# Optimization experiments

Measured on AMD Instinct MI355X. Metric: run time of the kernel, lower is better.

## Reference

```python
import jax, jax.numpy as jnp
import numpy as np

N_ITER = 2          # GenSP n_iter
M_COEF = 0.0        # GenSP M (positional-feature weight)
AFF_SOFTMAX = 1.0   # GenSP affinity_softmax


def setup_inputs() -> dict:
    key = jax.random.key(0)
    x = jax.random.normal(key, (2, 64, 256, 256), dtype=jnp.float32)
    return {"x": x, "stoken_size": 16}


def reference(x, stoken_size):
    # Faithful JAX version of GenSP.forward / ssn_iter (softmax_order='v0',
    # ws=None -> ws=2*stride0-1, i.e. each pixel searches its 9 neighboring
    # superpixel centroids; dist_type='l2' squared distance).
    B, C, H, W = x.shape
    s = int(stoken_size)
    nH, nW = (H - 1) // s + 1, (W - 1) // s + 1
    nS = nH * nW
    N = H * W

    # append_grid: concat scaled (y,x) coordinate channels, scale = M/stride0
    scale = jnp.asarray(M_COEF / s, x.dtype)
    gy, gx = jnp.meshgrid(jnp.arange(H, dtype=x.dtype) * scale,
                          jnp.arange(W, dtype=x.dtype) * scale, indexing='ij')
    grid = jnp.broadcast_to(jnp.stack([gy, gx])[None], (B, 2, H, W))
    feats = jnp.concatenate([x, grid], axis=1)          # [B, C+2, H, W]
    C2 = C + 2
    pf = feats.reshape(B, C2, N)                        # pixel features

    # calc_init_centroid: adaptive_avg_pool2d to (nH, nW); H,W divisible by s
    cent = feats.reshape(B, C2, nH, s, nW, s).mean(axis=(3, 5)).reshape(B, C2, nS)

    # per-pixel base superpixel cell and its 3x3 candidate neighborhood
    yy, xx = jnp.meshgrid(jnp.arange(H), jnp.arange(W), indexing='ij')
    sy = (yy // s).reshape(-1)                          # [N]
    sx = (xx // s).reshape(-1)
    dy, dx = jnp.meshgrid(jnp.arange(-1, 2), jnp.arange(-1, 2), indexing='ij')
    dy = dy.reshape(-1); dx = dx.reshape(-1)            # [9]
    cy = sy[:, None] + dy[None]                         # [N, 9]
    cx = sx[:, None] + dx[None]
    valid = (cy >= 0) & (cy < nH) & (cx >= 0) & (cx < nW)
    cand = jnp.where(valid, cy * nW + cx, 0)            # candidate spixel ids
    pix = jnp.broadcast_to(jnp.arange(N)[:, None], (N, 9))
    flat = (cand * N + pix).reshape(-1)                 # [9N] flat COO index
    NEG = jnp.asarray(-1e30, x.dtype)

    affinity = None
    for it in range(N_ITER):
        ck = cent[:, :, cand]                           # [B, C2, N, 9] gather
        d = jnp.sum((pf[:, :, :, None] - ck) ** 2, axis=1)  # squared-l2 [B,N,9]
        logits = jnp.where(valid[None], -AFF_SOFTMAX * d, NEG)
        w = jax.nn.softmax(logits, axis=-1)             # softmax_order 'v0'
        w = jnp.where(valid[None], w, jnp.asarray(0.0, x.dtype))
        # sparse-COO -> dense scatter: A[b, spix, pix] = w
        A = jnp.zeros((B, nS * N), x.dtype).at[:, flat].add(w.reshape(B, -1))
        affinity = A.reshape(B, nS, N)
        if it < N_ITER - 1:
            # spixel_features = bmm(A, pf^T) / (A.sum(2) + 1e-16)
            num = jnp.einsum('bsn,bcn->bcs', affinity, pf)
            den = affinity.sum(axis=2)[:, None] + 1e-16
            cent = num / den
    return affinity
```

## Files before the change

kernel.cpp:

```cpp
#include <hip/hip_runtime.h>
#include <cstdint>


#define WDIM   256
#define NPIX   65536
#define NSUP   256
#define OUT_F4 8388608u
#define WS_Z_F4 8320u

__device__ __forceinline__ unsigned short f2bf(float f) {
    unsigned u = __float_as_uint(f);
    u = (u + 0x7FFFu + ((u >> 16) & 1u)) >> 16;
    return (unsigned short)u;
}
__device__ __forceinline__ float bf2f(unsigned short h) {
    return __uint_as_float(((unsigned)h) << 16);
}

__global__ __launch_bounds__(256) void kfill(float4* __restrict__ out4,
                                             float4* __restrict__ ws4) {
    unsigned idx = blockIdx.x * 256u + threadIdx.x;
    float4 z = make_float4(0.f, 0.f, 0.f, 0.f);
    if (idx < OUT_F4) {
        out4[idx] = z;
    } else {
        unsigned k = idx - OUT_F4;
        if (k < WS_Z_F4) ws4[8192u + k] = z;
    }
}

__global__ __launch_bounds__(256) void kcent0(const float* __restrict__ x,
                                              float* __restrict__ cent0) {
    __shared__ float red[64];
    int blk = blockIdx.x;
    int b  = blk >> 10;
    int c  = (blk >> 4) & 63;
    int sy = blk & 15;
    const float4* s4 = (const float4*)(x + (((size_t)b << 22) | ((size_t)c << 16) | ((size_t)sy << 12)));
    int u = threadIdx.x;
    float4 a0 = s4[u], a1 = s4[u + 256], a2 = s4[u + 512], a3 = s4[u + 768];
    float p = (a0.x + a0.y + a0.z + a0.w) + (a1.x + a1.y + a1.z + a1.w)
            + (a2.x + a2.y + a2.z + a2.w) + (a3.x + a3.y + a3.z + a3.w);
    p += __shfl_xor(p, 1, 64);
    p += __shfl_xor(p, 2, 64);
    int lane = u & 63, wv = u >> 6;
    if ((lane & 3) == 0) red[wv * 16 + (lane >> 2)] = p;
    __syncthreads();
    if (u < 16) {
        float v = (red[u] + red[16 + u] + red[32 + u] + red[48 + u]) * (1.0f / 256.0f);
        cent0[(((b << 8) | (sy << 4) | u) << 6) + c] = v;
    }
}

__global__ __launch_bounds__(256) void kiter0(const float* __restrict__ x,
                                              const float* __restrict__ cent0,
                                              float* __restrict__ num,
                                              float* __restrict__ den) {
    __shared__ __align__(16) float smem[12544];
    float* w_lds = smem;
    unsigned short* pS = (unsigned short*)(smem + 3072);
    float* part = smem + 3072;

    int blk = blockIdx.x;
    int b = blk >> 8, sidx = blk & 255;
    int sy = sidx >> 4, sx = sidx & 15;
    int t  = threadIdx.x;
    int py = t >> 4, px = t & 15;
    int n  = ((sy << 4) + py) * WDIM + (sx << 4) + px;
    const float* xp = x + ((size_t)b << 22) + n;
    const float* cb = cent0 + ((size_t)b << 14);

    int candj[9]; bool valj[9];
#pragma unroll
    for (int j = 0; j < 9; j++) {
        int cy = sy + j / 3 - 1, cx = sx + j % 3 - 1;
        bool v = (cy >= 0) && (cy < 16) && (cx >= 0) && (cx < 16);
        valj[j] = v;
        candj[j] = v ? ((cy << 4) | cx) : 0;
    }

    float d[9];
#pragma unroll
    for (int j = 0; j < 9; j++) d[j] = 0.f;

#pragma unroll 8
    for (int cq = 0; cq < 32; cq++) {
        float pc0 = xp[(size_t)(2 * cq) << 16];
        float pc1 = xp[(size_t)(2 * cq + 1) << 16];
#pragma unroll
        for (int j = 0; j < 9; j++) {
            float c0 = cb[(candj[j] << 6) + 2 * cq];
            float c1 = cb[(candj[j] << 6) + 2 * cq + 1];
            float f0 = pc0 - c0, f1 = pc1 - c1;
            d[j] = fmaf(f0, f0, d[j]);
            d[j] = fmaf(f1, f1, d[j]);
        }
        *(ushort2*)&pS[t * 70 + 2 * cq] = make_ushort2(f2bf(pc0), f2bf(pc1));
    }

    float M = -1e30f;
#pragma unroll
    for (int j = 0; j < 9; j++) if (valj[j]) M = fmaxf(M, -d[j]);
    float w[9], Z = 0.f;
#pragma unroll
    for (int j = 0; j < 9; j++) { w[j] = valj[j] ? __expf(-d[j] - M) : 0.f; Z += w[j]; }
    float rZ = 1.0f / Z;
#pragma unroll
    for (int j = 0; j < 9; j++) { w[j] *= rZ; w_lds[t * 12 + j] = w[j]; }

    __syncthreads();

    int tg = t >> 4, cg = t & 15;
    float acc[9][4];
    float dacc[9];
#pragma unroll
    for (int j = 0; j < 9; j++) {
        dacc[j] = 0.f;
        acc[j][0] = 0.f; acc[j][1] = 0.f; acc[j][2] = 0.f; acc[j][3] = 0.f;
    }
#pragma unroll 4
    for (int i = 0; i < 16; i++) {
        int tt = (tg << 4) + i;
        float4 wA = *(const float4*)&w_lds[tt * 12];
        float4 wB = *(const float4*)&w_lds[tt * 12 + 4];
        float  w8 = w_lds[tt * 12 + 8];
        ushort2 A2 = *(const ushort2*)&pS[tt * 70 + 4 * cg];
        ushort2 B2 = *(const ushort2*)&pS[tt * 70 + 4 * cg + 2];
        float p0 = bf2f(A2.x), p1 = bf2f(A2.y), p2v = bf2f(B2.x), p3v = bf2f(B2.y);
        float ww[9] = {wA.x, wA.y, wA.z, wA.w, wB.x, wB.y, wB.z, wB.w, w8};
#pragma unroll
        for (int j = 0; j < 9; j++) {
            dacc[j] += ww[j];
            acc[j][0] = fmaf(ww[j], p0, acc[j][0]);
            acc[j][1] = fmaf(ww[j], p1, acc[j][1]);
            acc[j][2] = fmaf(ww[j], p2v, acc[j][2]);
            acc[j][3] = fmaf(ww[j], p3v, acc[j][3]);
        }
    }

    __syncthreads();

#pragma unroll
    for (int j = 0; j < 9; j++)
        *(float4*)&part[tg * 592 + (j << 6) + (cg << 2)] =
            make_float4(acc[j][0], acc[j][1], acc[j][2], acc[j][3]);
    if (cg == 0) {
#pragma unroll
        for (int j = 0; j < 9; j++) part[tg * 592 + 576 + j] = dacc[j];
    }

    __syncthreads();

    for (int o = t; o < 585; o += 256) {
        float s = 0.f;
#pragma unroll
        for (int tg2 = 0; tg2 < 16; tg2++) s += part[tg2 * 592 + o];
        if (o < 576) {
            int j = o >> 6, c = o & 63;
            int cy = sy + j / 3 - 1, cx = sx + j % 3 - 1;
            if (cy >= 0 && cy < 16 && cx >= 0 && cx < 16)
                atomicAdd(&num[((size_t)((b << 8) | (cy << 4) | cx) << 6) + c], s);
        } else {
            int j = o - 576;
            int cy = sy + j / 3 - 1, cx = sx + j % 3 - 1;
            if (cy >= 0 && cy < 16 && cx >= 0 && cx < 16)
                atomicAdd(&den[(b << 8) | (cy << 4) | cx], s);
        }
    }
}

__global__ __launch_bounds__(256) void kdiv(const float* __restrict__ num,
                                            const float* __restrict__ den,
                                            float* __restrict__ cent1) {
    int i = blockIdx.x * 256 + threadIdx.x;
    cent1[i] = num[i] / (den[i >> 6] + 1e-16f);
}

__global__ __launch_bounds__(256) void kiter1(const float* __restrict__ x,
                                              const float* __restrict__ cent1,
                                              float* __restrict__ out) {
    int blk = blockIdx.x;
    int b = blk >> 8, sidx = blk & 255;
    int sy = sidx >> 4, sx = sidx & 15;
    int t  = threadIdx.x;
    int py = t >> 4, px = t & 15;
    int n  = ((sy << 4) + py) * WDIM + (sx << 4) + px;
    const float* xp = x + ((size_t)b << 22) + n;
    const float* cb = cent1 + ((size_t)b << 14);

    int candj[9]; bool valj[9];
#pragma unroll
    for (int j = 0; j < 9; j++) {
        int cy = sy + j / 3 - 1, cx = sx + j % 3 - 1;
        bool v = (cy >= 0) && (cy < 16) && (cx >= 0) && (cx < 16);
        valj[j] = v;
        candj[j] = v ? ((cy << 4) | cx) : 0;
    }

    float d[9];
#pragma unroll
    for (int j = 0; j < 9; j++) d[j] = 0.f;

#pragma unroll 8
    for (int cq = 0; cq < 32; cq++) {
        float pc0 = xp[(size_t)(2 * cq) << 16];
        float pc1 = xp[(size_t)(2 * cq + 1) << 16];
#pragma unroll
        for (int j = 0; j < 9; j++) {
            float c0 = cb[(candj[j] << 6) + 2 * cq];
            float c1 = cb[(candj[j] << 6) + 2 * cq + 1];
            float f0 = pc0 - c0, f1 = pc1 - c1;
            d[j] = fmaf(f0, f0, d[j]);
            d[j] = fmaf(f1, f1, d[j]);
        }
    }

    float M = -1e30f;
#pragma unroll
    for (int j = 0; j < 9; j++) if (valj[j]) M = fmaxf(M, -d[j]);
    float w[9], Z = 0.f;
#pragma unroll
    for (int j = 0; j < 9; j++) { w[j] = valj[j] ? __expf(-d[j] - M) : 0.f; Z += w[j]; }
    float rZ = 1.0f / Z;

    float* ob = out + ((size_t)b << 24) + n;
#pragma unroll
    for (int j = 0; j < 9; j++)
        if (valj[j]) ob[(size_t)candj[j] << 16] = w[j] * rZ;
}

extern "C" void kernel_launch(void* const* d_in, const int* in_sizes, int n_in,
                              void* d_out, int out_size, void* d_ws, size_t ws_size,
                              hipStream_t stream) {
    (void)in_sizes; (void)n_in; (void)out_size; (void)ws_size;
    const float* x = (const float*)d_in[0];
    float* out = (float*)d_out;
    float* ws  = (float*)d_ws;
    float* cent0 = ws;
    float* num   = ws + 32768;
    float* den   = ws + 65536;
    float* cent1 = ws + 66048;

    kfill <<<32801, 256, 0, stream>>>((float4*)out, (float4*)ws);
    kcent0<<<2048,  256, 0, stream>>>(x, cent0);
    kiter0<<<512,   256, 0, stream>>>(x, cent0, num, den);
    kdiv  <<<128,   256, 0, stream>>>(num, den, cent1);
    kiter1<<<512,   256, 0, stream>>>(x, cent1, out);
}
```

Baseline: 189.5 us.

## Replace zero-fill plus scatter with compact weights and single dense expand pass

Result: no change. 189.3 us (-0.1%).

```diff
diff --git a/kernel.cpp b/kernel.cpp
--- a/kernel.cpp
+++ b/kernel.cpp
@@ -1,12 +1,6 @@
 #include <hip/hip_runtime.h>
 #include <cstdint>
 
-
-#define WDIM   256
-#define NPIX   65536
-#define NSUP   256
-#define OUT_F4 8388608u
-#define WS_Z_F4 8320u
 
 __device__ __forceinline__ unsigned short f2bf(float f) {
     unsigned u = __float_as_uint(f);
@@ -17,27 +11,17 @@
     return __uint_as_float(((unsigned)h) << 16);
 }
 
-__global__ __launch_bounds__(256) void kfill(float4* __restrict__ out4,
-                                             float4* __restrict__ ws4) {
-    unsigned idx = blockIdx.x * 256u + threadIdx.x;
-    float4 z = make_float4(0.f, 0.f, 0.f, 0.f);
-    if (idx < OUT_F4) {
-        out4[idx] = z;
-    } else {
-        unsigned k = idx - OUT_F4;
-        if (k < WS_Z_F4) ws4[8192u + k] = z;
-    }
-}
-
 __global__ __launch_bounds__(256) void kcent0(const float* __restrict__ x,
-                                              float* __restrict__ cent0) {
+                                              float* __restrict__ cent0,
+                                              float* __restrict__ numden) {
     __shared__ float red[64];
     int blk = blockIdx.x;
+    int u = threadIdx.x;
+    if (blk < 130) numden[blk * 256 + u] = 0.f;
     int b  = blk >> 10;
     int c  = (blk >> 4) & 63;
     int sy = blk & 15;
     const float4* s4 = (const float4*)(x + (((size_t)b << 22) | ((size_t)c << 16) | ((size_t)sy << 12)));
-    int u = threadIdx.x;
     float4 a0 = s4[u], a1 = s4[u + 256], a2 = s4[u + 512], a3 = s4[u + 768];
     float p = (a0.x + a0.y + a0.z + a0.w) + (a1.x + a1.y + a1.z + a1.w)
             + (a2.x + a2.y + a2.z + a2.w) + (a3.x + a3.y + a3.z + a3.w);
@@ -56,17 +40,18 @@
                                               const float* __restrict__ cent0,
                                               float* __restrict__ num,
                                               float* __restrict__ den) {
-    __shared__ __align__(16) float smem[12544];
-    float* w_lds = smem;
-    unsigned short* pS = (unsigned short*)(smem + 3072);
-    float* part = smem + 3072;
+    __shared__ __align__(16) float smem[12608];
+    float* kc    = smem;
+    float* w_lds = smem + 576;
+    unsigned short* pS = (unsigned short*)(smem + 3648);
+    float* part  = smem + 576;
 
     int blk = blockIdx.x;
     int b = blk >> 8, sidx = blk & 255;
     int sy = sidx >> 4, sx = sidx & 15;
     int t  = threadIdx.x;
     int py = t >> 4, px = t & 15;
-    int n  = ((sy << 4) + py) * WDIM + (sx << 4) + px;
+    int n  = ((sy << 4) + py) * 256 + (sx << 4) + px;
     const float* xp = x + ((size_t)b << 22) + n;
     const float* cb = cent0 + ((size_t)b << 14);
 
@@ -79,23 +64,32 @@
         candj[j] = v ? ((cy << 4) | cx) : 0;
     }
 
+    for (int idx = t; idx < 576; idx += 256) {
+        int j = idx >> 6, c = idx & 63;
+        kc[idx] = cb[(candj[j] << 6) + c];
+    }
+    __syncthreads();
+
     float d[9];
 #pragma unroll
     for (int j = 0; j < 9; j++) d[j] = 0.f;
-
-#pragma unroll 8
-    for (int cq = 0; cq < 32; cq++) {
-        float pc0 = xp[(size_t)(2 * cq) << 16];
-        float pc1 = xp[(size_t)(2 * cq + 1) << 16];
+#pragma unroll
+    for (int c = 0; c < 64; c += 4) {
+        float p0 = xp[(size_t)(c + 0) << 16];
+        float p1 = xp[(size_t)(c + 1) << 16];
+        float p2 = xp[(size_t)(c + 2) << 16];
+        float p3 = xp[(size_t)(c + 3) << 16];
 #pragma unroll
         for (int j = 0; j < 9; j++) {
-            float c0 = cb[(candj[j] << 6) + 2 * cq];
-            float c1 = cb[(candj[j] << 6) + 2 * cq + 1];
-            float f0 = pc0 - c0, f1 = pc1 - c1;
+            float4 k4 = *(const float4*)&kc[(j << 6) + c];
+            float f0 = p0 - k4.x, f1 = p1 - k4.y, f2 = p2 - k4.z, f3 = p3 - k4.w;
             d[j] = fmaf(f0, f0, d[j]);
             d[j] = fmaf(f1, f1, d[j]);
-        }
-        *(ushort2*)&pS[t * 70 + 2 * cq] = make_ushort2(f2bf(pc0), f2bf(pc1));
+            d[j] = fmaf(f2, f2, d[j]);
+            d[j] = fmaf(f3, f3, d[j]);
+        }
+        *(ushort2*)&pS[t * 70 + c]     = make_ushort2(f2bf(p0), f2bf(p1));
+        *(ushort2*)&pS[t * 70 + c + 2] = make_ushort2(f2bf(p2), f2bf(p3));
     }
 
     float M = -1e30f;
@@ -176,15 +170,16 @@
     cent1[i] = num[i] / (den[i >> 6] + 1e-16f);
 }
 
-__global__ __launch_bounds__(256) void kiter1(const float* __restrict__ x,
-                                              const float* __restrict__ cent1,
-                                              float* __restrict__ out) {
+__global__ __launch_bounds__(256) void kweights(const float* __restrict__ x,
+                                                const float* __restrict__ cent1,
+                                                float* __restrict__ W) {
+    __shared__ __align__(16) float kc[576];
     int blk = blockIdx.x;
     int b = blk >> 8, sidx = blk & 255;
     int sy = sidx >> 4, sx = sidx & 15;
     int t  = threadIdx.x;
     int py = t >> 4, px = t & 15;
-    int n  = ((sy << 4) + py) * WDIM + (sx << 4) + px;
+    int n  = ((sy << 4) + py) * 256 + (sx << 4) + px;
     const float* xp = x + ((size_t)b << 22) + n;
     const float* cb = cent1 + ((size_t)b << 14);
 
@@ -197,21 +192,29 @@
         candj[j] = v ? ((cy << 4) | cx) : 0;
     }
 
+    for (int idx = t; idx < 576; idx += 256) {
+        int j = idx >> 6, c = idx & 63;
+        kc[idx] = cb[(candj[j] << 6) + c];
+    }
+    __syncthreads();
+
     float d[9];
 #pragma unroll
     for (int j = 0; j < 9; j++) d[j] = 0.f;
-
-#pragma unroll 8
-    for (int cq = 0; cq < 32; cq++) {
-        float pc0 = xp[(size_t)(2 * cq) << 16];
-        float pc1 = xp[(size_t)(2 * cq + 1) << 16];
+#pragma unroll
+    for (int c = 0; c < 64; c += 4) {
+        float p0 = xp[(size_t)(c + 0) << 16];
+        float p1 = xp[(size_t)(c + 1) << 16];
+        float p2 = xp[(size_t)(c + 2) << 16];
+        float p3 = xp[(size_t)(c + 3) << 16];
 #pragma unroll
         for (int j = 0; j < 9; j++) {
-            float c0 = cb[(candj[j] << 6) + 2 * cq];
-            float c1 = cb[(candj[j] << 6) + 2 * cq + 1];
-            float f0 = pc0 - c0, f1 = pc1 - c1;
+            float4 k4 = *(const float4*)&kc[(j << 6) + c];
+            float f0 = p0 - k4.x, f1 = p1 - k4.y, f2 = p2 - k4.z, f3 = p3 - k4.w;
             d[j] = fmaf(f0, f0, d[j]);
             d[j] = fmaf(f1, f1, d[j]);
+            d[j] = fmaf(f2, f2, d[j]);
+            d[j] = fmaf(f3, f3, d[j]);
         }
     }
 
@@ -223,10 +226,32 @@
     for (int j = 0; j < 9; j++) { w[j] = valj[j] ? __expf(-d[j] - M) : 0.f; Z += w[j]; }
     float rZ = 1.0f / Z;
 
-    float* ob = out + ((size_t)b << 24) + n;
+    float* wb = W + (((size_t)b * 9) << 16) + n;
 #pragma unroll
     for (int j = 0; j < 9; j++)
-        if (valj[j]) ob[(size_t)candj[j] << 16] = w[j] * rZ;
+        if (valj[j]) wb[(size_t)j << 16] = w[j] * rZ;
+}
+
+__global__ __launch_bounds__(256) void kexpand(const float4* __restrict__ W4,
+                                               float4* __restrict__ out4) {
+    unsigned g0 = blockIdx.x * 256u + threadIdx.x;
+#pragma unroll
+    for (int it = 0; it < 4; it++) {
+        unsigned g = g0 + (unsigned)it * 2097152u;
+        unsigned b = g >> 22;
+        unsigned s = (g >> 14) & 255u;
+        unsigned q = g & 16383u;
+        int syn = (int)(q >> 10);
+        int sxn = (int)((q >> 2) & 15u);
+        int dy = (int)(s >> 4)  - syn;
+        int dx = (int)(s & 15u) - sxn;
+        float4 v = make_float4(0.f, 0.f, 0.f, 0.f);
+        if (dy >= -1 && dy <= 1 && dx >= -1 && dx <= 1) {
+            int j = (dy + 1) * 3 + (dx + 1);
+            v = W4[(((size_t)b * 9 + j) << 14) + q];
+        }
+        out4[g] = v;
+    }
 }
 
 extern "C" void kernel_launch(void* const* d_in, const int* in_sizes, int n_in,
@@ -240,10 +265,11 @@
     float* num   = ws + 32768;
     float* den   = ws + 65536;
     float* cent1 = ws + 66048;
-
-    kfill <<<32801, 256, 0, stream>>>((float4*)out, (float4*)ws);
-    kcent0<<<2048,  256, 0, stream>>>(x, cent0);
-    kiter0<<<512,   256, 0, stream>>>(x, cent0, num, den);
-    kdiv  <<<128,   256, 0, stream>>>(num, den, cent1);
-    kiter1<<<512,   256, 0, stream>>>(x, cent1, out);
-}
+    float* W     = ws + 98816;
+
+    kcent0  <<<2048, 256, 0, stream>>>(x, cent0, num);
+    kiter0  <<<512,  256, 0, stream>>>(x, cent0, num, den);
+    kdiv    <<<128,  256, 0, stream>>>(num, den, cent1);
+    kweights<<<512,  256, 0, stream>>>(x, cent1, W);
+    kexpand <<<8192, 256, 0, stream>>>((const float4*)W, (float4*)out);
+}
```
